# Performance work log

Hardware: AMD Instinct MI355X
Metric: run time of the kernel (lower is better)

## Reference

```python
import jax, jax.numpy as jnp
import numpy as np
from jax import lax

N_CFG = [[4, 4]]
D_CFG = [4, 8, 8]
B, H, W_IMG = 64, 32, 32


def _make_idx(N=N_CFG, D=D_CFG):
    """Replicates CNNModel.createConnectivity and converts each layer's sparse
    connectivity rows into a dense [node, fan_in] gather-index array (all rows in a
    layer have equal fan-in for these factorizations)."""
    N_ = int(np.prod(N[0]))
    I = np.eye(N_)
    Wm = []
    for n in N:
        v = 1
        for n_ in n:
            w = np.zeros((N_, N_))
            for k in range(n_):
                w = w + np.roll(I, axis=0, shift=k * v)
            Wm.append(w)
            v = v * n_
    conn = [np.kron(np.ones((D[i + 1], D[i])), Wm[i]) for i in range(len(Wm))]
    nodes = [int(d) * N_ for d in D]
    conn.insert(0, np.ones((nodes[0], 3)))
    idx = []
    for c in conn:
        rows = [np.nonzero(c[k])[0] for k in range(c.shape[0])]
        idx.append(jnp.asarray(np.stack(rows), dtype=jnp.int32))
    return idx, nodes

IDX, NODES = _make_idx()  # fan-ins: 3, 16, 32; nodes: 64, 128, 128


def setup_inputs() -> dict:
    key = jax.random.key(0)
    ks = jax.random.split(key, 11)
    nrm = lambda k, s: (jax.random.normal(k, s, jnp.float32) * 0.05)
    return {
        "inputs": jax.random.normal(ks[0], (B, H, W_IMG, 3), jnp.float32),
        "cw0": nrm(ks[1], (3, 3, 3, NODES[0])),
        "cb0": nrm(ks[2], (NODES[0],)),
        "cw1": nrm(ks[3], (3, 3, 16, NODES[1])),
        "cb1": nrm(ks[4], (NODES[1],)),
        "cw2": nrm(ks[5], (3, 3, 32, NODES[2])),
        "cb2": nrm(ks[6], (NODES[2],)),
        "dw1": nrm(ks[7], (H * W_IMG * NODES[2], 50)),
        "db1": nrm(ks[8], (50,)),
        "dw2": nrm(ks[9], (50, 10)),
        "db2": nrm(ks[10], (10,)),
    }


def _sparse_layer(x, idx, w, b):
    # x: [B,H,W,C_prev]; idx: [node, F]; w: [3,3,F,node]; b: [node]
    # Gather each node's fan-in channels, then run all per-node 1-filter 3x3 convs
    # as a single grouped convolution (feature_group_count = node).
    node, F = idx.shape
    g = x[..., idx.reshape(-1)]  # [B,H,W,node*F]
    y = lax.conv_general_dilated(
        g, w, window_strides=(1, 1), padding="SAME",
        dimension_numbers=("NHWC", "HWIO", "NHWC"),
        feature_group_count=node)  # [B,H,W,node]
    return jax.nn.relu(y + b)


def reference(inputs, cw0, cb0, cw1, cb1, cw2, cb2, dw1, db1, dw2, db2):
    x = inputs.reshape(-1, H, W_IMG, 3)
    x = _sparse_layer(x, IDX[0], cw0, cb0)
    x = _sparse_layer(x, IDX[1], cw1, cb1)
    x = _sparse_layer(x, IDX[2], cw2, cb2)
    x = x.reshape(x.shape[0], -1)  # Flatten (NHWC row-major, matches TF)
    x = jax.nn.relu(x @ dw1 + db1)
    return jax.nn.softmax(x @ dw2 + db2, axis=-1)
```

## Files before the change

kernel.cpp:

```cpp
#include <hip/hip_runtime.h>
#include <math.h>

typedef unsigned short u16;
typedef unsigned int u32;
typedef __attribute__((ext_vector_type(8))) short short8v;
typedef __attribute__((ext_vector_type(4))) float f32x4;

#define X0PN_OFF 4734976
#define X2B_OFF  7102464
#define H2_OFF   2200000
#define W1Q_OFF  11300000
#define W2P_OFF  11330000

__device__ __forceinline__ u16 f2bf(float f) {
    union { float f; u32 i; } c; c.f = f;
    u32 r = c.i + 0x7fffu + ((c.i >> 16) & 1u);
    return (u16)(r >> 16);
}
__device__ __forceinline__ int Sf(int i0, int m) {
    return (i0 >= 3) ? (i0 - 3 + m) : ((m <= i0) ? m : (12 + m));
}

__global__ __launch_bounds__(256) void prep_l0(const float* __restrict__ cw1,
    const float* __restrict__ cw2, const float* __restrict__ in,
    const float* __restrict__ cw0, const float* __restrict__ cb0,
    u16* __restrict__ x0pn, u16* __restrict__ x1pn,
    u16* __restrict__ w1q, u16* __restrict__ w2p) {
    int bi = blockIdx.x;
    if (bi < 1080) {
        int t = bi * 256 + threadIdx.x;
        if (t < 202752) {
            uint4 z = {0u, 0u, 0u, 0u};
            int cell, v; u16* base; int nch;
            if (t < 67584) { v = t & 7; cell = t >> 3; base = x0pn; nch = 64; }
            else { int u = t - 67584; v = u & 15; cell = u >> 4; base = x1pn; nch = 128; }
            int b = cell / 132, ci = cell - b * 132;
            int y, x;
            if (ci < 34)       { y = 0;       x = ci; }
            else if (ci < 68)  { y = 33;      x = ci - 34; }
            else if (ci < 100) { y = ci - 67; x = 0; }
            else               { y = ci - 99; x = 33; }
            *(uint4*)(base + ((b * 34 + y) * 34 + x) * nch + v * 8) = z;
            return;
        }
        int u0 = t - 202752;
        if (u0 < 36864) {
            int j = u0 & 7, lane = (u0 >> 3) & 63;
            int tp = u0 >> 9;
            int tap = tp % 9, pr = tp / 9;
            int n = lane & 15;
            int k = 8 * (lane >> 4) + j;
            float v = 0.f;
            if (n < 8) {
                if (k < 16) {
                    int f = 4 * (k & 3) + (k >> 2);
                    v = cw1[(tap * 16 + f) * 128 + 2 * pr + 16 * n];
                }
            } else {
                if (k >= 16) {
                    int k2 = k - 16;
                    int f = 4 * (k2 & 3) + (k2 >> 2);
                    v = cw1[(tap * 16 + f) * 128 + 2 * pr + 1 + 16 * (n - 8)];
                }
            }
            w1q[u0] = f2bf(v);
        } else {
            int u = u0 - 36864;
            int j = u & 7, lane = (u >> 3) & 63;
            int nt = (u >> 9) & 1;
            int gt = u >> 10, tap = gt % 9, g = gt / 9;
            int k = 8 * (lane >> 4) + j;
            int f = 4 * (k >> 2) + (k & 3);
            int n = g + 4 * (nt * 16 + (lane & 15));
            w2p[u] = f2bf(cw2[(tap * 32 + f) * 128 + n]);
        }
        return;
    }
    int lb = bi - 1080;
    int b = lb >> 2, qt = lb & 3;
    int t = threadIdx.x, lane = t & 63, wv = t >> 6;
    int col = lane & 15, khi = lane >> 4;

    short8v Bf[4];
#pragma unroll
    for (int nb = 0; nb < 4; ++nb) {
        union { short8v v; u16 e[8]; } B;
#pragma unroll
        for (int j = 0; j < 8; ++j) {
            int k = 8 * khi + j;
            B.e[j] = (k < 27) ? f2bf(cw0[k * 64 + nb * 16 + col]) : (u16)0;
        }
        Bf[nb] = B.v;
    }
    float bias[4];
#pragma unroll
    for (int nb = 0; nb < 4; ++nb) bias[nb] = cb0[nb * 16 + col];

    for (int it = 0; it < 4; ++it) {
        int tile = qt * 16 + wv * 4 + it;
        int py = tile >> 1, px0 = (tile & 1) * 16;
        union { short8v v; u16 e[8]; } A;
#pragma unroll
        for (int j = 0; j < 8; ++j) {
            int k = 8 * khi + j;
            float v = 0.f;
            if (k < 27) {
                int tap = k / 3, c = k - 3 * tap;
                int dy = tap / 3, dx = tap - 3 * dy;
                int y = py + dy - 1, x = px0 + col + dx - 1;
                if ((unsigned)y < 32u && (unsigned)x < 32u)
                    v = in[((b * 32 + y) * 32 + x) * 3 + c];
            }
            A.e[j] = f2bf(v);
        }
        f32x4 acc[4];
#pragma unroll
        for (int nb = 0; nb < 4; ++nb) {
            f32x4 ci = {bias[nb], bias[nb], bias[nb], bias[nb]};
            acc[nb] = __builtin_amdgcn_mfma_f32_16x16x32_bf16(A.v, Bf[nb], ci, 0, 0, 0);
        }
#pragma unroll
        for (int r = 0; r < 4; ++r) {
            int px_l = 4 * khi + r;
            u32 lo = (u32)f2bf(fmaxf(acc[0][r], 0.f)) | ((u32)f2bf(fmaxf(acc[1][r], 0.f)) << 16);
            u32 hi = (u32)f2bf(fmaxf(acc[2][r], 0.f)) | ((u32)f2bf(fmaxf(acc[3][r], 0.f)) << 16);
            uint2 pk = {lo, hi};
            *(uint2*)(x0pn + ((size_t)(b * 34 + py + 1) * 34 + px0 + px_l + 1) * 64 + 4 * col) = pk;
        }
    }
}

__global__ __launch_bounds__(256) void l1_mfma(const u16* __restrict__ x0pn,
    const u16* __restrict__ w1q, const float* __restrict__ cb1, u16* __restrict__ x1pn) {
    __shared__ __align__(16) unsigned char x0s[26112];
    int bi = blockIdx.x;
    int xcd = bi & 7, slot = bi >> 3;
    int b = xcd * 8 + (slot >> 4);
    int rem = slot & 15;
    int rq = rem >> 1, pp = rem & 1;
    int t = threadIdx.x, lane = t & 63, wv = t >> 6;

    {
        const u16* src = x0pn + (size_t)(b * 1156 + rq * 136) * 64;
        for (int c = t; c < 1632; c += 256) {
            uint4 v = *(const uint4*)(src + c * 8);
            int p = c >> 3;
            int dst = (c * 16) ^ ((p & 7) << 4);
            *(uint4*)(x0s + dst) = v;
        }
    }
    __syncthreads();

    int col = lane & 15, khi = lane >> 4;

    int pr = pp * 4 + wv;
    int i0a = 2 * pr, i0b = 2 * pr + 1;
    int i0g = (khi >= 2) ? i0b : i0a;
    int mb = 2 * (khi & 1);
    int o0 = 8 * Sf(i0g, mb), o1 = 8 * Sf(i0g, mb + 1);

    short8v wf[9];
#pragma unroll
    for (int tap = 0; tap < 9; ++tap)
        wf[tap] = *(const short8v*)(w1q + ((pr * 9 + tap) * 64 + lane) * 8);

    int node = (col < 8) ? (i0a + 16 * col) : (i0b + 16 * (col - 8));
    float bv = cb1[node];
    int cperm = 32 * (node & 3) + (node >> 2);

    for (int mt = 0; mt < 8; ++mt) {
        int row_l = mt >> 1, cbase = (mt & 1) * 16;
        f32x4 acc = {bv, bv, bv, bv};
        int pbase = row_l * 34 + cbase + col;
#pragma unroll
        for (int tap = 0; tap < 9; ++tap) {
            const int dy = tap / 3, dx = tap % 3;
            int p = pbase + dy * 34 + dx;
            int sw = (p & 7) << 4;
            int base = p * 128;
            union { short8v v; uint2 h[2]; } A;
            A.h[0] = *(const uint2*)(x0s + base + (o0 ^ sw));
            A.h[1] = *(const uint2*)(x0s + base + (o1 ^ sw));
            acc = __builtin_amdgcn_mfma_f32_16x16x32_bf16(A.v, wf[tap], acc, 0, 0, 0);
        }
        int prow = rq * 4 + row_l + 1;
        u16* ob = x1pn + ((size_t)(b * 34 + prow) * 34) * 128 + cperm;
#pragma unroll
        for (int r = 0; r < 4; ++r) {
            int pcol = cbase + khi * 4 + r + 1;
            ob[pcol * 128] = f2bf(fmaxf(acc[r], 0.f));
        }
    }
}

__global__ __launch_bounds__(256) void l2_mfma(const u16* __restrict__ x1pn,
    const u16* __restrict__ w2p, const float* __restrict__ cb2, u16* __restrict__ x2b) {
    __shared__ __align__(16) u16 x1s[6 * 34 * 32];
    int bi = blockIdx.x;
    int xcd = bi & 7, slot = bi >> 3;
    int b = xcd * 8 + (slot >> 5);
    int rem = slot & 31;
    int rq = rem >> 2, g = rem & 3;
    int t = threadIdx.x, lane = t & 63, wvi = t >> 6;
    int col = lane & 15, khi = lane >> 4;

    {
        const u16* src = x1pn + (size_t)(b * 34 + rq * 4) * (34 * 128) + g * 32;
        for (int c = t; c < 816; c += 256) {
            int row = c / 136, e = c - row * 136;
            int px = e >> 2, part = e & 3;
            uint4 v = *(const uint4*)(src + (size_t)row * (34 * 128) + px * 128 + part * 8);
            *(uint4*)(x1s + (row * 34 + px) * 32 + part * 8) = v;
        }
    }
    __syncthreads();

    short8v wf[9][2];
#pragma unroll
    for (int tap = 0; tap < 9; ++tap)
#pragma unroll
        for (int nt = 0; nt < 2; ++nt)
            wf[tap][nt] = *(const short8v*)(w2p + (((g * 9 + tap) * 2 + nt) * 64 + lane) * 8);

    float bv0 = cb2[g + 4 * col];
    float bv1 = cb2[g + 4 * (16 + col)];

    int y = rq * 4 + wvi;
    f32x4 acc[2][2];
    acc[0][0] = (f32x4){bv0, bv0, bv0, bv0}; acc[0][1] = (f32x4){bv1, bv1, bv1, bv1};
    acc[1][0] = acc[0][0];                   acc[1][1] = acc[0][1];
#pragma unroll
    for (int tap = 0; tap < 9; ++tap) {
        const int dy = tap / 3, dx = tap % 3;
#pragma unroll
        for (int ms = 0; ms < 2; ++ms) {
            int px = (wvi + dy) * 34 + ms * 16 + col + dx;
            short8v a = *(const short8v*)(x1s + px * 32 + khi * 8);
            acc[ms][0] = __builtin_amdgcn_mfma_f32_16x16x32_bf16(a, wf[tap][0], acc[ms][0], 0, 0, 0);
            acc[ms][1] = __builtin_amdgcn_mfma_f32_16x16x32_bf16(a, wf[tap][1], acc[ms][1], 0, 0, 0);
        }
    }
#pragma unroll
    for (int ms = 0; ms < 2; ++ms)
#pragma unroll
        for (int nt = 0; nt < 2; ++nt) {
#pragma unroll
            for (int r = 0; r < 4; ++r) {
                int px = ms * 16 + 4 * khi + r;
                x2b[(size_t)b * 131072 + ((g * 2 + nt) * 1024 + y * 32 + px) * 16 + col]
                    = f2bf(fmaxf(acc[ms][nt][r], 0.f));
            }
        }
}

#define D1_NB 512
__global__ __launch_bounds__(256) void d1_mfma(const u16* __restrict__ x2b,
                                               const float* __restrict__ dw1,
                                               float* __restrict__ partial) {
    int kb = blockIdx.x;
    int t = threadIdx.x, lane = t & 63, w = t >> 6;
    int col = lane & 15, khi = lane >> 4;
    int n = 16 * w + col;
    f32x4 acc[4];
#pragma unroll
    for (int m = 0; m < 4; ++m) acc[m] = (f32x4){0.f, 0.f, 0.f, 0.f};

    int k0 = kb * 256;
#pragma unroll 2
    for (int ks = 0; ks < 8; ++ks) {
        int kbase = k0 + ks * 32 + 8 * khi;
        int c0 = kbase & 15;
        int q = kbase >> 4;
        int g = q >> 11, nt = (q >> 10) & 1, pix = q & 1023;
        union { short8v v; u16 e[8]; } Bf;
        if (n < 50) {
            const float* wp = dw1 + (size_t)(pix * 128 + g + 64 * nt + 4 * c0) * 50 + n;
#pragma unroll
            for (int j = 0; j < 8; ++j) Bf.e[j] = f2bf(wp[j * 200]);
        } else {
            Bf.v = (short8v)0;
        }
#pragma unroll
        for (int m = 0; m < 4; ++m) {
            short8v A = *(const short8v*)(x2b + (size_t)(m * 16 + col) * 131072 + kbase);
            acc[m] = __builtin_amdgcn_mfma_f32_16x16x32_bf16(A, Bf.v, acc[m], 0, 0, 0);
        }
    }
    float* po = partial + kb * 4096;
#pragma unroll
    for (int m = 0; m < 4; ++m)
#pragma unroll
        for (int r = 0; r < 4; ++r)
            po[(m * 16 + khi * 4 + r) * 64 + n] = acc[m][r];
}

__global__ __launch_bounds__(256) void d1_reduce(const float* __restrict__ partial,
                                                 float* __restrict__ h2) {
    __shared__ float sm[4][64];
    int bi = blockIdx.x;
    int t = threadIdx.x;
    int tt = t & 63, pp = t >> 6;
    int idx = bi * 64 + tt;
    float s0 = 0.f, s1 = 0.f, s2 = 0.f, s3 = 0.f;
    int base = pp * 128;
    for (int cb = 0; cb < 128; cb += 4) {
        s0 += partial[(size_t)(base + cb + 0) * 4096 + idx];
        s1 += partial[(size_t)(base + cb + 1) * 4096 + idx];
        s2 += partial[(size_t)(base + cb + 2) * 4096 + idx];
        s3 += partial[(size_t)(base + cb + 3) * 4096 + idx];
    }
    sm[pp][tt] = (s0 + s1) + (s2 + s3);
    __syncthreads();
    if (pp == 0)
        h2[idx] = (sm[0][tt] + sm[1][tt]) + (sm[2][tt] + sm[3][tt]);
}

__global__ void d2_kernel(const float* __restrict__ h2, const float* __restrict__ db1,
                          const float* __restrict__ dw2, const float* __restrict__ db2,
                          float* __restrict__ out) {
    int b = threadIdx.x;
    float a[10];
#pragma unroll
    for (int j = 0; j < 10; ++j) a[j] = db2[j];
    for (int i = 0; i < 50; ++i) {
        float v = fmaxf(h2[b * 64 + i] + db1[i], 0.f);
#pragma unroll
        for (int j = 0; j < 10; ++j) a[j] += v * dw2[i * 10 + j];
    }
    float mx = a[0];
#pragma unroll
    for (int j = 1; j < 10; ++j) mx = fmaxf(mx, a[j]);
    float s = 0.f;
#pragma unroll
    for (int j = 0; j < 10; ++j) { a[j] = expf(a[j] - mx); s += a[j]; }
    float inv = 1.f / s;
#pragma unroll
    for (int j = 0; j < 10; ++j) out[b * 10 + j] = a[j] * inv;
}

extern "C" void kernel_launch(void* const* d_in, const int* in_sizes, int n_in,
                              void* d_out, int out_size, void* d_ws, size_t ws_size,
                              hipStream_t stream) {
    const float* inputs = (const float*)d_in[0];
    const float* cw0 = (const float*)d_in[1];
    const float* cb0 = (const float*)d_in[2];
    const float* cw1 = (const float*)d_in[3];
    const float* cb1 = (const float*)d_in[4];
    const float* cw2 = (const float*)d_in[5];
    const float* cb2 = (const float*)d_in[6];
    const float* dw1 = (const float*)d_in[7];
    const float* db1 = (const float*)d_in[8];
    const float* dw2 = (const float*)d_in[9];
    const float* db2 = (const float*)d_in[10];
    float* out = (float*)d_out;

    float* ws = (float*)d_ws;
    u16* x1pn = (u16*)ws;
    u16* x0pn = (u16*)(ws + X0PN_OFF);
    u16* x2b  = (u16*)(ws + X2B_OFF);
    float* partial = ws;
    float* h2 = ws + H2_OFF;
    u16* w1q  = (u16*)(ws + W1Q_OFF);
    u16* w2p  = (u16*)(ws + W2P_OFF);

    prep_l0<<<1336, 256, 0, stream>>>(cw1, cw2, inputs, cw0, cb0, x0pn, x1pn, w1q, w2p);
    l1_mfma<<<1024, 256, 0, stream>>>(x0pn, w1q, cb1, x1pn);
    l2_mfma<<<2048, 256, 0, stream>>>(x1pn, w2p, cb2, x2b);
    d1_mfma<<<D1_NB, 256, 0, stream>>>(x2b, dw1, partial);
    d1_reduce<<<64, 256, 0, stream>>>(partial, h2);
    d2_kernel<<<1, 64, 0, stream>>>(h2, db1, dw2, db2, out);
}
```

Baseline: 76.21 us.

## Pre-transpose dense weights to bf16 and fuse reduce with final dense layer

The prep kernel gains extra blocks that convert dw1 from fp32 to bf16 and transpose it into a K-contiguous layout per output column. d1_mfma can then load B fragments with one 16-byte vector load instead of eight strided fp32 loads plus conversions. The partial-sum reduction and the final dense+softmax are merged into one 64-block kernel, which removes a launch and the serial single-block d2 step. The cost is a transpose pass over the 26MB dw1 on every call and its extra writes.

```diff
diff --git a/kernel.cpp b/kernel.cpp
--- a/kernel.cpp
+++ b/kernel.cpp
@@ -8,9 +8,9 @@
 
 #define X0PN_OFF 4734976
 #define X2B_OFF  7102464
-#define H2_OFF   2200000
 #define W1Q_OFF  11300000
 #define W2P_OFF  11330000
+#define DW1T_OFF 12000000
 
 __device__ __forceinline__ u16 f2bf(float f) {
     union { float f; u32 i; } c; c.f = f;
@@ -24,9 +24,26 @@
 __global__ __launch_bounds__(256) void prep_l0(const float* __restrict__ cw1,
     const float* __restrict__ cw2, const float* __restrict__ in,
     const float* __restrict__ cw0, const float* __restrict__ cb0,
+    const float* __restrict__ dw1,
     u16* __restrict__ x0pn, u16* __restrict__ x1pn,
-    u16* __restrict__ w1q, u16* __restrict__ w2p) {
+    u16* __restrict__ w1q, u16* __restrict__ w2p, u16* __restrict__ dw1t) {
     int bi = blockIdx.x;
+    if (bi >= 1336) {
+        int u = (bi - 1336) * 256 + threadIdx.x;
+        int c0 = u & 15;
+        int q = (u >> 4) & 8191;
+        int jc = u >> 17;
+        int g = q >> 11, nt = (q >> 10) & 1, pix = q & 1023;
+        int row = pix * 128 + g + 4 * (nt * 16 + c0);
+        int klin = q * 16 + c0;
+        const float* src = dw1 + (size_t)row * 50 + jc * 8;
+#pragma unroll
+        for (int jj = 0; jj < 8; ++jj) {
+            int j = jc * 8 + jj;
+            if (j < 50) dw1t[(size_t)j * 131072 + klin] = f2bf(src[jj]);
+        }
+        return;
+    }
     if (bi < 1080) {
         int t = bi * 256 + threadIdx.x;
         if (t < 202752) {
@@ -255,7 +272,7 @@
 
 #define D1_NB 512
 __global__ __launch_bounds__(256) void d1_mfma(const u16* __restrict__ x2b,
-                                               const float* __restrict__ dw1,
+                                               const u16* __restrict__ dw1t,
                                                float* __restrict__ partial) {
     int kb = blockIdx.x;
     int t = threadIdx.x, lane = t & 63, w = t >> 6;
@@ -266,24 +283,18 @@
     for (int m = 0; m < 4; ++m) acc[m] = (f32x4){0.f, 0.f, 0.f, 0.f};
 
     int k0 = kb * 256;
+    const u16* brow = dw1t + (size_t)n * 131072;
+    bool nv = (n < 50);
 #pragma unroll 2
     for (int ks = 0; ks < 8; ++ks) {
         int kbase = k0 + ks * 32 + 8 * khi;
-        int c0 = kbase & 15;
-        int q = kbase >> 4;
-        int g = q >> 11, nt = (q >> 10) & 1, pix = q & 1023;
-        union { short8v v; u16 e[8]; } Bf;
-        if (n < 50) {
-            const float* wp = dw1 + (size_t)(pix * 128 + g + 64 * nt + 4 * c0) * 50 + n;
-#pragma unroll
-            for (int j = 0; j < 8; ++j) Bf.e[j] = f2bf(wp[j * 200]);
-        } else {
-            Bf.v = (short8v)0;
-        }
+        short8v Bv;
+        if (nv) Bv = *(const short8v*)(brow + kbase);
+        else    Bv = (short8v)0;
 #pragma unroll
         for (int m = 0; m < 4; ++m) {
             short8v A = *(const short8v*)(x2b + (size_t)(m * 16 + col) * 131072 + kbase);
-            acc[m] = __builtin_amdgcn_mfma_f32_16x16x32_bf16(A, Bf.v, acc[m], 0, 0, 0);
+            acc[m] = __builtin_amdgcn_mfma_f32_16x16x32_bf16(A, Bv, acc[m], 0, 0, 0);
         }
     }
     float* po = partial + kb * 4096;
@@ -294,48 +305,47 @@
             po[(m * 16 + khi * 4 + r) * 64 + n] = acc[m][r];
 }
 
-__global__ __launch_bounds__(256) void d1_reduce(const float* __restrict__ partial,
-                                                 float* __restrict__ h2) {
+__global__ __launch_bounds__(256) void rd2_kernel(const float* __restrict__ partial,
+    const float* __restrict__ db1, const float* __restrict__ dw2,
+    const float* __restrict__ db2, float* __restrict__ out) {
     __shared__ float sm[4][64];
-    int bi = blockIdx.x;
+    __shared__ float hs[64];
+    __shared__ float as[10];
+    int b = blockIdx.x;
     int t = threadIdx.x;
-    int tt = t & 63, pp = t >> 6;
-    int idx = bi * 64 + tt;
+    int j = t & 63, pp = t >> 6;
     float s0 = 0.f, s1 = 0.f, s2 = 0.f, s3 = 0.f;
     int base = pp * 128;
     for (int cb = 0; cb < 128; cb += 4) {
-        s0 += partial[(size_t)(base + cb + 0) * 4096 + idx];
-        s1 += partial[(size_t)(base + cb + 1) * 4096 + idx];
-        s2 += partial[(size_t)(base + cb + 2) * 4096 + idx];
-        s3 += partial[(size_t)(base + cb + 3) * 4096 + idx];
-    }
-    sm[pp][tt] = (s0 + s1) + (s2 + s3);
-    __syncthreads();
-    if (pp == 0)
-        h2[idx] = (sm[0][tt] + sm[1][tt]) + (sm[2][tt] + sm[3][tt]);
-}
-
-__global__ void d2_kernel(const float* __restrict__ h2, const float* __restrict__ db1,
-                          const float* __restrict__ dw2, const float* __restrict__ db2,
-                          float* __restrict__ out) {
-    int b = threadIdx.x;
-    float a[10];
-#pragma unroll
-    for (int j = 0; j < 10; ++j) a[j] = db2[j];
-    for (int i = 0; i < 50; ++i) {
-        float v = fmaxf(h2[b * 64 + i] + db1[i], 0.f);
-#pragma unroll
-        for (int j = 0; j < 10; ++j) a[j] += v * dw2[i * 10 + j];
-    }
-    float mx = a[0];
-#pragma unroll
-    for (int j = 1; j < 10; ++j) mx = fmaxf(mx, a[j]);
-    float s = 0.f;
-#pragma unroll
-    for (int j = 0; j < 10; ++j) { a[j] = expf(a[j] - mx); s += a[j]; }
-    float inv = 1.f / s;
-#pragma unroll
-    for (int j = 0; j < 10; ++j) out[b * 10 + j] = a[j] * inv;
+        s0 += partial[(size_t)(base + cb + 0) * 4096 + b * 64 + j];
+        s1 += partial[(size_t)(base + cb + 1) * 4096 + b * 64 + j];
+        s2 += partial[(size_t)(base + cb + 2) * 4096 + b * 64 + j];
+        s3 += partial[(size_t)(base + cb + 3) * 4096 + b * 64 + j];
+    }
+    sm[pp][j] = (s0 + s1) + (s2 + s3);
+    __syncthreads();
+    if (pp == 0) {
+        float h = (sm[0][j] + sm[1][j]) + (sm[2][j] + sm[3][j]);
+        hs[j] = (j < 50) ? fmaxf(h + db1[j], 0.f) : 0.f;
+    }
+    __syncthreads();
+    if (t < 10) {
+        float a = db2[t];
+        for (int i = 0; i < 50; ++i) a += hs[i] * dw2[i * 10 + t];
+        as[t] = a;
+    }
+    __syncthreads();
+    if (t == 0) {
+        float mx = as[0];
+#pragma unroll
+        for (int q = 1; q < 10; ++q) mx = fmaxf(mx, as[q]);
+        float e[10], s = 0.f;
+#pragma unroll
+        for (int q = 0; q < 10; ++q) { e[q] = expf(as[q] - mx); s += e[q]; }
+        float inv = 1.f / s;
+#pragma unroll
+        for (int q = 0; q < 10; ++q) out[b * 10 + q] = e[q] * inv;
+    }
 }
 
 extern "C" void kernel_launch(void* const* d_in, const int* in_sizes, int n_in,
@@ -359,14 +369,14 @@
     u16* x0pn = (u16*)(ws + X0PN_OFF);
     u16* x2b  = (u16*)(ws + X2B_OFF);
     float* partial = ws;
-    float* h2 = ws + H2_OFF;
     u16* w1q  = (u16*)(ws + W1Q_OFF);
     u16* w2p  = (u16*)(ws + W2P_OFF);
-
-    prep_l0<<<1336, 256, 0, stream>>>(cw1, cw2, inputs, cw0, cb0, x0pn, x1pn, w1q, w2p);
+    u16* dw1t = (u16*)(ws + DW1T_OFF);
+
+    prep_l0<<<4920, 256, 0, stream>>>(cw1, cw2, inputs, cw0, cb0, dw1,
+                                      x0pn, x1pn, w1q, w2p, dw1t);
     l1_mfma<<<1024, 256, 0, stream>>>(x0pn, w1q, cb1, x1pn);
     l2_mfma<<<2048, 256, 0, stream>>>(x1pn, w2p, cb2, x2b);
-    d1_mfma<<<D1_NB, 256, 0, stream>>>(x2b, dw1, partial);
-    d1_reduce<<<64, 256, 0, stream>>>(partial, h2);
-    d2_kernel<<<1, 64, 0, stream>>>(h2, db1, dw2, db2, out);
-}
+    d1_mfma<<<D1_NB, 256, 0, stream>>>(x2b, dw1t, partial);
+    rd2_kernel<<<64, 256, 0, stream>>>(partial, db1, dw2, db2, out);
+}
```

Measured after the change: 86.05 us. 1.13x slower.
